# Kernel tuning notes

Hardware: AMD Instinct MI355X
Metric: run time of the kernel (lower is better)

The kernel has to match this reference:

```python
import jax, jax.numpy as jnp
import numpy as np

B, D_MODEL, D_MEM, H, N_MEM = 128, 1024, 64, 16, 4096


def setup_inputs() -> dict:
    key = jax.random.key(0)
    ks = jax.random.split(key, 6)
    scale = 1.0 / np.sqrt(D_MODEL)
    return {
        "query": jax.random.normal(ks[0], (B, D_MODEL), jnp.float32),
        "addresses": jax.random.normal(ks[1], (N_MEM, D_MEM), jnp.float32),
        "memories": jax.random.normal(ks[2], (B, N_MEM, D_MEM), jnp.float32),
        "Wq": jax.random.normal(ks[3], (D_MODEL, D_MODEL), jnp.float32) * scale,
        "bq": jnp.zeros((D_MODEL,), jnp.float32),
        "Wm": jax.random.normal(ks[4], (D_MODEL, D_MODEL), jnp.float32) * scale,
        "bm": jnp.zeros((D_MODEL,), jnp.float32),
    }


def reference(query, addresses, memories, Wq, bq, Wm, bm):
    # query projection -> heads: (B, H, d_mem)
    q = (query @ Wq.T + bq).reshape(B, H, D_MEM)
    # stage 1: build linear-attention kernel over the memory-slot dim
    k = jax.nn.relu(memories + addresses)            # (B, N, d_mem)
    matrix = jnp.einsum('bnd,bne->bde', k, memories)  # (B, d_mem, d_mem)
    normalizer = jnp.sum(k, axis=-2)                  # (B, d_mem)
    # stage 2: read the kernel with activated queries
    qa = jax.nn.relu(q)                               # (B, H, d_mem)
    numerator = jnp.einsum('bhd,bde->bhe', qa, matrix)
    denominator = jnp.einsum('bhd,bd->bh', qa, normalizer)[..., None] + 1e-5
    attn = numerator / denominator                    # (B, H, d_mem)
    return attn.reshape(B, H * D_MEM) @ Wm.T + bm     # (B, d_model)
```

## Files before the change

kernel.cpp:

```cpp
#include <hip/hip_runtime.h>
#include <hip/hip_bf16.h>

#define BATCH 128
#define DMEM 64
#define NMEM 4096
#define DMODEL 1024
#define S1 4
#define LDS_STRIDE 40

typedef __bf16 v8bf __attribute__((ext_vector_type(8)));
typedef __bf16 v2bf __attribute__((ext_vector_type(2)));
typedef float v4f __attribute__((ext_vector_type(4)));
typedef float v16f __attribute__((ext_vector_type(16)));

__device__ __forceinline__ void gemm_sk(const float* __restrict__ A,
                                        const float* __restrict__ W,
                                        float* __restrict__ dst,
                                        int m0, int n0, int k0,
                                        float* smem) {
    float(*As)[36] = (float(*)[36])smem;
    float(*Ws)[36] = (float(*)[36])(smem + 32 * 36);
    const int t = threadIdx.x;
    const int lrow = t >> 3;
    const int lc4 = (t & 7) * 4;
    const int rp = t >> 4;
    const int cp = t & 15;

    float acc00 = 0.f, acc01 = 0.f, acc10 = 0.f, acc11 = 0.f;

    v4f av = *(const v4f*)&A[(size_t)(m0 + lrow) * DMODEL + k0 + lc4];
    v4f wv = *(const v4f*)&W[(size_t)(n0 + lrow) * DMODEL + k0 + lc4];

    for (int c = 0; c < 4; ++c) {
        __syncthreads();
        *(v4f*)&As[lrow][lc4] = av;
        *(v4f*)&Ws[lrow][lc4] = wv;
        __syncthreads();
        if (c + 1 < 4) {
            const int kc = k0 + (c + 1) * 32;
            av = *(const v4f*)&A[(size_t)(m0 + lrow) * DMODEL + kc + lc4];
            wv = *(const v4f*)&W[(size_t)(n0 + lrow) * DMODEL + kc + lc4];
        }
#pragma unroll
        for (int kk = 0; kk < 32; kk += 4) {
            v4f a0 = *(v4f*)&As[rp][kk];
            v4f a1 = *(v4f*)&As[rp + 16][kk];
            v4f b0 = *(v4f*)&Ws[cp][kk];
            v4f b1 = *(v4f*)&Ws[cp + 16][kk];
#pragma unroll
            for (int q = 0; q < 4; ++q) {
                acc00 = fmaf(a0[q], b0[q], acc00);
                acc01 = fmaf(a0[q], b1[q], acc01);
                acc10 = fmaf(a1[q], b0[q], acc10);
                acc11 = fmaf(a1[q], b1[q], acc11);
            }
        }
    }
    dst[(size_t)(m0 + rp) * DMODEL + n0 + cp] = acc00;
    dst[(size_t)(m0 + rp) * DMODEL + n0 + cp + 16] = acc01;
    dst[(size_t)(m0 + rp + 16) * DMODEL + n0 + cp] = acc10;
    dst[(size_t)(m0 + rp + 16) * DMODEL + n0 + cp + 16] = acc11;
}

__global__ __launch_bounds__(256, 3) void k1(const float* __restrict__ mem,
                                             const float* __restrict__ addr,
                                             float* __restrict__ pmat,
                                             float* __restrict__ pnorm,
                                             const float* __restrict__ query,
                                             const float* __restrict__ Wq,
                                             float* __restrict__ qa_p) {
    __shared__ __align__(16) char smem[24576];
    const int bid = blockIdx.x;
    const int nst = BATCH * S1;

    if (bid >= nst) {
        const int b2 = bid - nst;
        const int m0 = (b2 & 3) * 32;
        const int n0 = ((b2 >> 2) & 31) * 32;
        const int ks = b2 >> 7;
        gemm_sk(query, Wq, qa_p + (size_t)ks * BATCH * DMODEL,
                m0, n0, ks * 128, (float*)smem);
        return;
    }

    float* norm_s = (float*)(smem + 20480);

    const int t = threadIdx.x;
    const int b = bid & (BATCH - 1);
    const int s = bid >> 7;
    const int slots_per = NMEM / S1;
    const int chunks = slots_per >> 5;

    const int u = t & 15;
    const int v = t >> 4;
    const int d0 = u * 4;

    const int l = t & 63;
    const int wv = t >> 6;
    const int strip = wv >> 1;
    const int kh = wv & 1;
    const int lrow = l & 31;
    const int lh = l >> 5;

    const size_t mem_base = ((size_t)b * NMEM + (size_t)s * slots_per) * DMEM;
    const size_t addr_base = (size_t)s * slots_per * DMEM;
    const size_t so = (size_t)(2 * v) * DMEM + d0;

    v16f acc0, acc1;
#pragma unroll
    for (int r = 0; r < 16; ++r) { acc0[r] = 0.f; acc1[r] = 0.f; }
    float nacc[4] = {0.f, 0.f, 0.f, 0.f};

    v4f mE0 = *(const v4f*)&mem[mem_base + so];
    v4f mE1 = *(const v4f*)&mem[mem_base + so + DMEM];
    v4f aE0 = *(const v4f*)&addr[addr_base + so];
    v4f aE1 = *(const v4f*)&addr[addr_base + so + DMEM];
    v4f mO0 = *(const v4f*)&mem[mem_base + 2048 + so];
    v4f mO1 = *(const v4f*)&mem[mem_base + 2048 + so + DMEM];
    v4f aO0 = *(const v4f*)&addr[addr_base + 2048 + so];
    v4f aO1 = *(const v4f*)&addr[addr_base + 2048 + so + DMEM];

    __bf16* kb0 = (__bf16*)smem;
    __bf16* mb0 = kb0 + 64 * LDS_STRIDE;
    __bf16* kb1 = (__bf16*)(smem + 10240);
    __bf16* mb1 = kb1 + 64 * LDS_STRIDE;
    const int cb = 16 * kh + 8 * lh;

    for (int cc = 0; cc < chunks; cc += 2) {
#pragma unroll
        for (int i = 0; i < 4; ++i) {
            float kf0 = fmaxf(mE0[i] + aE0[i], 0.f);
            float kf1 = fmaxf(mE1[i] + aE1[i], 0.f);
            nacc[i] += kf0 + kf1;
            v2bf kp; kp[0] = (__bf16)kf0; kp[1] = (__bf16)kf1;
            v2bf mp; mp[0] = (__bf16)mE0[i]; mp[1] = (__bf16)mE1[i];
            *(v2bf*)&kb0[(d0 + i) * LDS_STRIDE + 2 * v] = kp;
            *(v2bf*)&mb0[(d0 + i) * LDS_STRIDE + 2 * v] = mp;
        }
        if (cc + 2 < chunks) {
            const size_t coff = (size_t)(cc + 2) * 32 * DMEM;
            mE0 = *(const v4f*)&mem[mem_base + coff + so];
            mE1 = *(const v4f*)&mem[mem_base + coff + so + DMEM];
            aE0 = *(const v4f*)&addr[addr_base + coff + so];
            aE1 = *(const v4f*)&addr[addr_base + coff + so + DMEM];
        }
        __syncthreads();
        {
            v8bf af = *(v8bf*)&kb0[(32 * strip + lrow) * LDS_STRIDE + cb];
            v8bf b0 = *(v8bf*)&mb0[lrow * LDS_STRIDE + cb];
            v8bf b1 = *(v8bf*)&mb0[(32 + lrow) * LDS_STRIDE + cb];
            acc0 = __builtin_amdgcn_mfma_f32_32x32x16_bf16(af, b0, acc0, 0, 0, 0);
            acc1 = __builtin_amdgcn_mfma_f32_32x32x16_bf16(af, b1, acc1, 0, 0, 0);
        }
#pragma unroll
        for (int i = 0; i < 4; ++i) {
            float kf0 = fmaxf(mO0[i] + aO0[i], 0.f);
            float kf1 = fmaxf(mO1[i] + aO1[i], 0.f);
            nacc[i] += kf0 + kf1;
            v2bf kp; kp[0] = (__bf16)kf0; kp[1] = (__bf16)kf1;
            v2bf mp; mp[0] = (__bf16)mO0[i]; mp[1] = (__bf16)mO1[i];
            *(v2bf*)&kb1[(d0 + i) * LDS_STRIDE + 2 * v] = kp;
            *(v2bf*)&mb1[(d0 + i) * LDS_STRIDE + 2 * v] = mp;
        }
        if (cc + 3 < chunks) {
            const size_t coff = (size_t)(cc + 3) * 32 * DMEM;
            mO0 = *(const v4f*)&mem[mem_base + coff + so];
            mO1 = *(const v4f*)&mem[mem_base + coff + so + DMEM];
            aO0 = *(const v4f*)&addr[addr_base + coff + so];
            aO1 = *(const v4f*)&addr[addr_base + coff + so + DMEM];
        }
        __syncthreads();
        {
            v8bf af = *(v8bf*)&kb1[(32 * strip + lrow) * LDS_STRIDE + cb];
            v8bf b0 = *(v8bf*)&mb1[lrow * LDS_STRIDE + cb];
            v8bf b1 = *(v8bf*)&mb1[(32 + lrow) * LDS_STRIDE + cb];
            acc0 = __builtin_amdgcn_mfma_f32_32x32x16_bf16(af, b0, acc0, 0, 0, 0);
            acc1 = __builtin_amdgcn_mfma_f32_32x32x16_bf16(af, b1, acc1, 0, 0, 0);
        }
    }

    __syncthreads();
    float* red = (float*)smem;
#pragma unroll
    for (int i = 0; i < 4; ++i) norm_s[v * 64 + d0 + i] = nacc[i];
    if (kh == 1) {
#pragma unroll
        for (int r = 0; r < 16; ++r) {
            int row = (r & 3) + 8 * (r >> 2) + 4 * lh;
            int d = 32 * strip + row;
            red[lrow * 68 + d] = acc0[r];
            red[(32 + lrow) * 68 + d] = acc1[r];
        }
    }
    __syncthreads();
    if (kh == 0) {
#pragma unroll
        for (int r = 0; r < 16; ++r) {
            int row = (r & 3) + 8 * (r >> 2) + 4 * lh;
            int d = 32 * strip + row;
            red[lrow * 68 + d] += acc0[r];
            red[(32 + lrow) * 68 + d] += acc1[r];
        }
    }
    __syncthreads();
    {
        float* pm = pmat + ((size_t)s * BATCH + b) * 4096;
        const int e = t >> 2;
        const int ds = (t & 3) * 16;
#pragma unroll
        for (int j = 0; j < 4; ++j)
            *(v4f*)&pm[e * 64 + ds + 4 * j] = *(v4f*)&red[e * 68 + ds + 4 * j];
    }
    if (t < 64) {
        float ssum = 0.f;
#pragma unroll
        for (int g = 0; g < 16; ++g) ssum += norm_s[g * 64 + t];
        pnorm[((size_t)s * BATCH + b) * 64 + t] = ssum;
    }
}

__global__ __launch_bounds__(256) void stage2(const float* __restrict__ pmat,
                                              const float* __restrict__ pnorm,
                                              const float* __restrict__ qa_p,
                                              const float* __restrict__ bq,
                                              float* __restrict__ attn) {
    __shared__ float mat_s[16 * 68];
    __shared__ float qa_s[16 * 68];
    __shared__ float nrm_s[64];
    const int t = threadIdx.x;
    const int b = blockIdx.x >> 2;
    const int eq = blockIdx.x & 3;

    {
        const int i4 = t * 4;
        v4f acc = (v4f){0.f, 0.f, 0.f, 0.f};
#pragma unroll
        for (int s = 0; s < S1; ++s)
            acc += *(const v4f*)&pmat[((size_t)s * BATCH + b) * 4096 + eq * 1024 + i4];
        *(v4f*)&mat_s[(i4 >> 6) * 68 + (i4 & 63)] = acc;
    }
#pragma unroll
    for (int i = 0; i < 4; ++i) {
        const int idx = t + 256 * i;
        float ssum = 0.f;
#pragma unroll
        for (int ks = 0; ks < 8; ++ks)
            ssum += qa_p[((size_t)ks * BATCH + b) * DMODEL + idx];
        qa_s[(idx >> 6) * 68 + (idx & 63)] = fmaxf(ssum + bq[idx], 0.f);
    }
    if (t < 64) {
        float ssum = 0.f;
#pragma unroll
        for (int s = 0; s < S1; ++s)
            ssum += pnorm[((size_t)s * BATCH + b) * 64 + t];
        nrm_s[t] = ssum;
    }
    __syncthreads();

    const int h = t >> 4;
    const int e = t & 15;
    float num = 0.f, den = 0.f;
#pragma unroll 8
    for (int d = 0; d < 64; ++d) {
        float q = qa_s[h * 68 + d];
        num = fmaf(q, mat_s[e * 68 + d], num);
        den = fmaf(q, nrm_s[d], den);
    }
    attn[(size_t)b * DMODEL + h * 64 + eq * 16 + e] = num / (den + 1e-5f);
}

__global__ __launch_bounds__(256) void gemm_out(const float* __restrict__ A,
                                                const float* __restrict__ W,
                                                float* __restrict__ out_p) {
    __shared__ __align__(16) float smem[2 * 32 * 36];
    const int ks = blockIdx.z;
    gemm_sk(A, W, out_p + (size_t)ks * BATCH * DMODEL,
            blockIdx.x * 32, blockIdx.y * 32, ks * 128, smem);
}

__global__ __launch_bounds__(256) void combine(const float* __restrict__ out_p,
                                               const float* __restrict__ bm,
                                               float* __restrict__ out) {
    const int i = blockIdx.x * 256 + threadIdx.x;
    float ssum = bm[i & (DMODEL - 1)];
#pragma unroll
    for (int ks = 0; ks < 8; ++ks)
        ssum += out_p[(size_t)ks * BATCH * DMODEL + i];
    out[i] = ssum;
}

extern "C" void kernel_launch(void* const* d_in, const int* in_sizes, int n_in,
                              void* d_out, int out_size, void* d_ws, size_t ws_size,
                              hipStream_t stream) {
    const float* query     = (const float*)d_in[0];
    const float* addresses = (const float*)d_in[1];
    const float* memories  = (const float*)d_in[2];
    const float* Wq        = (const float*)d_in[3];
    const float* bq        = (const float*)d_in[4];
    const float* Wm        = (const float*)d_in[5];
    const float* bm        = (const float*)d_in[6];
    float* out = (float*)d_out;
    float* ws = (float*)d_ws;

    float* qa_p    = ws;
    float* attn_ws = qa_p + 1048576;
    float* pnorm   = attn_ws + 131072;
    float* pmat    = pnorm + 32768;
    float* out_p   = pmat + 2097152;

    k1<<<dim3(BATCH * S1 + 1024), 256, 0, stream>>>(memories, addresses, pmat,
                                                    pnorm, query, Wq, qa_p);
    stage2<<<dim3(512), 256, 0, stream>>>(pmat, pnorm, qa_p, bq, attn_ws);
    gemm_out<<<dim3(4, 32, 8), 256, 0, stream>>>(attn_ws, Wm, out_p);
    combine<<<dim3(512), 256, 0, stream>>>(out_p, bm, out);
}
```

Measured before the change: 226.8 us.

## Use 64x64 register-tiled GEMM, drop split-K for query projection, fuse bias+relu

Replaces the 32x32 tile GEMM helper with a 64x64 tile, 4x4 per-thread register-blocked version that double-buffers LDS across two chunk buffers. The query projection inside k1 now runs as 32 full-K blocks that write qa directly with bias and ReLU applied, instead of 1024 split-K blocks writing 8 partial sums that stage2 had to reduce. The output GEMM uses the same helper with fewer, larger blocks. This cuts partial-sum traffic and raises arithmetic intensity. The cost is that the projection now sits on only 32 long full-K blocks, which may lengthen k1's tail, and k1 needs more LDS per block.

```diff
diff --git a/kernel.cpp b/kernel.cpp
--- a/kernel.cpp
+++ b/kernel.cpp
@@ -13,53 +13,101 @@
 typedef float v4f __attribute__((ext_vector_type(4)));
 typedef float v16f __attribute__((ext_vector_type(16)));
 
-__device__ __forceinline__ void gemm_sk(const float* __restrict__ A,
-                                        const float* __restrict__ W,
-                                        float* __restrict__ dst,
-                                        int m0, int n0, int k0,
-                                        float* smem) {
-    float(*As)[36] = (float(*)[36])smem;
-    float(*Ws)[36] = (float(*)[36])(smem + 32 * 36);
+__device__ __forceinline__ void gemm64(const float* __restrict__ A,
+                                       const float* __restrict__ W,
+                                       const float* __restrict__ bias,
+                                       float* __restrict__ dst,
+                                       int m0, int n0, int k0, int nchunks,
+                                       int relu, float* smem) {
+    float* As0 = smem;
+    float* Ws0 = smem + 64 * 36;
+    float* As1 = smem + 2 * 64 * 36;
+    float* Ws1 = smem + 3 * 64 * 36;
     const int t = threadIdx.x;
-    const int lrow = t >> 3;
-    const int lc4 = (t & 7) * 4;
+    const int lrow = t >> 2;
+    const int lc8 = (t & 3) * 8;
     const int rp = t >> 4;
     const int cp = t & 15;
 
-    float acc00 = 0.f, acc01 = 0.f, acc10 = 0.f, acc11 = 0.f;
-
-    v4f av = *(const v4f*)&A[(size_t)(m0 + lrow) * DMODEL + k0 + lc4];
-    v4f wv = *(const v4f*)&W[(size_t)(n0 + lrow) * DMODEL + k0 + lc4];
-
-    for (int c = 0; c < 4; ++c) {
+    float acc[4][4];
+#pragma unroll
+    for (int i = 0; i < 4; ++i)
+#pragma unroll
+        for (int j = 0; j < 4; ++j) acc[i][j] = 0.f;
+
+    const float* Arow = A + (size_t)(m0 + lrow) * DMODEL + lc8;
+    const float* Wrow = W + (size_t)(n0 + lrow) * DMODEL + lc8;
+
+    v4f aE0 = *(const v4f*)&Arow[k0];
+    v4f aE1 = *(const v4f*)&Arow[k0 + 4];
+    v4f wE0 = *(const v4f*)&Wrow[k0];
+    v4f wE1 = *(const v4f*)&Wrow[k0 + 4];
+    v4f aO0 = *(const v4f*)&Arow[k0 + 32];
+    v4f aO1 = *(const v4f*)&Arow[k0 + 36];
+    v4f wO0 = *(const v4f*)&Wrow[k0 + 32];
+    v4f wO1 = *(const v4f*)&Wrow[k0 + 36];
+
+    for (int cc = 0; cc < nchunks; cc += 2) {
+        *(v4f*)&As0[lrow * 36 + lc8] = aE0;
+        *(v4f*)&As0[lrow * 36 + lc8 + 4] = aE1;
+        *(v4f*)&Ws0[lrow * 36 + lc8] = wE0;
+        *(v4f*)&Ws0[lrow * 36 + lc8 + 4] = wE1;
+        if (cc + 2 < nchunks) {
+            const int kc = k0 + (cc + 2) * 32;
+            aE0 = *(const v4f*)&Arow[kc]; aE1 = *(const v4f*)&Arow[kc + 4];
+            wE0 = *(const v4f*)&Wrow[kc]; wE1 = *(const v4f*)&Wrow[kc + 4];
+        }
         __syncthreads();
-        *(v4f*)&As[lrow][lc4] = av;
-        *(v4f*)&Ws[lrow][lc4] = wv;
+#pragma unroll
+        for (int kk = 0; kk < 32; kk += 4) {
+            v4f a[4], b[4];
+#pragma unroll
+            for (int i = 0; i < 4; ++i) a[i] = *(v4f*)&As0[(rp + 16 * i) * 36 + kk];
+#pragma unroll
+            for (int j = 0; j < 4; ++j) b[j] = *(v4f*)&Ws0[(cp + 16 * j) * 36 + kk];
+#pragma unroll
+            for (int i = 0; i < 4; ++i)
+#pragma unroll
+                for (int j = 0; j < 4; ++j)
+#pragma unroll
+                    for (int q = 0; q < 4; ++q)
+                        acc[i][j] = fmaf(a[i][q], b[j][q], acc[i][j]);
+        }
+        *(v4f*)&As1[lrow * 36 + lc8] = aO0;
+        *(v4f*)&As1[lrow * 36 + lc8 + 4] = aO1;
+        *(v4f*)&Ws1[lrow * 36 + lc8] = wO0;
+        *(v4f*)&Ws1[lrow * 36 + lc8 + 4] = wO1;
+        if (cc + 3 < nchunks) {
+            const int kc = k0 + (cc + 3) * 32;
+            aO0 = *(const v4f*)&Arow[kc]; aO1 = *(const v4f*)&Arow[kc + 4];
+            wO0 = *(const v4f*)&Wrow[kc]; wO1 = *(const v4f*)&Wrow[kc + 4];
+        }
         __syncthreads();
-        if (c + 1 < 4) {
-            const int kc = k0 + (c + 1) * 32;
-            av = *(const v4f*)&A[(size_t)(m0 + lrow) * DMODEL + kc + lc4];
-            wv = *(const v4f*)&W[(size_t)(n0 + lrow) * DMODEL + kc + lc4];
-        }
 #pragma unroll
         for (int kk = 0; kk < 32; kk += 4) {
-            v4f a0 = *(v4f*)&As[rp][kk];
-            v4f a1 = *(v4f*)&As[rp + 16][kk];
-            v4f b0 = *(v4f*)&Ws[cp][kk];
-            v4f b1 = *(v4f*)&Ws[cp + 16][kk];
-#pragma unroll
-            for (int q = 0; q < 4; ++q) {
-                acc00 = fmaf(a0[q], b0[q], acc00);
-                acc01 = fmaf(a0[q], b1[q], acc01);
-                acc10 = fmaf(a1[q], b0[q], acc10);
-                acc11 = fmaf(a1[q], b1[q], acc11);
-            }
-        }
-    }
-    dst[(size_t)(m0 + rp) * DMODEL + n0 + cp] = acc00;
-    dst[(size_t)(m0 + rp) * DMODEL + n0 + cp + 16] = acc01;
-    dst[(size_t)(m0 + rp + 16) * DMODEL + n0 + cp] = acc10;
-    dst[(size_t)(m0 + rp + 16) * DMODEL + n0 + cp + 16] = acc11;
+            v4f a[4], b[4];
+#pragma unroll
+            for (int i = 0; i < 4; ++i) a[i] = *(v4f*)&As1[(rp + 16 * i) * 36 + kk];
+#pragma unroll
+            for (int j = 0; j < 4; ++j) b[j] = *(v4f*)&Ws1[(cp + 16 * j) * 36 + kk];
+#pragma unroll
+            for (int i = 0; i < 4; ++i)
+#pragma unroll
+                for (int j = 0; j < 4; ++j)
+#pragma unroll
+                    for (int q = 0; q < 4; ++q)
+                        acc[i][j] = fmaf(a[i][q], b[j][q], acc[i][j]);
+        }
+    }
+
+#pragma unroll
+    for (int i = 0; i < 4; ++i)
+#pragma unroll
+        for (int j = 0; j < 4; ++j) {
+            float o = acc[i][j] + (bias ? bias[n0 + cp + 16 * j] : 0.f);
+            if (relu) o = fmaxf(o, 0.f);
+            dst[(size_t)(m0 + rp + 16 * i) * DMODEL + n0 + cp + 16 * j] = o;
+        }
 }
 
 __global__ __launch_bounds__(256, 3) void k1(const float* __restrict__ mem,
@@ -68,18 +116,16 @@
                                              float* __restrict__ pnorm,
                                              const float* __restrict__ query,
                                              const float* __restrict__ Wq,
-                                             float* __restrict__ qa_p) {
-    __shared__ __align__(16) char smem[24576];
+                                             const float* __restrict__ bq,
+                                             float* __restrict__ qa) {
+    __shared__ __align__(16) char smem[36864];
     const int bid = blockIdx.x;
     const int nst = BATCH * S1;
 
     if (bid >= nst) {
         const int b2 = bid - nst;
-        const int m0 = (b2 & 3) * 32;
-        const int n0 = ((b2 >> 2) & 31) * 32;
-        const int ks = b2 >> 7;
-        gemm_sk(query, Wq, qa_p + (size_t)ks * BATCH * DMODEL,
-                m0, n0, ks * 128, (float*)smem);
+        gemm64(query, Wq, bq, qa, (b2 & 1) * 64, (b2 >> 1) * 64, 0, 32, 1,
+               (float*)smem);
         return;
     }
 
@@ -221,8 +267,7 @@
 
 __global__ __launch_bounds__(256) void stage2(const float* __restrict__ pmat,
                                               const float* __restrict__ pnorm,
-                                              const float* __restrict__ qa_p,
-                                              const float* __restrict__ bq,
+                                              const float* __restrict__ qa,
                                               float* __restrict__ attn) {
     __shared__ float mat_s[16 * 68];
     __shared__ float qa_s[16 * 68];
@@ -242,11 +287,7 @@
 #pragma unroll
     for (int i = 0; i < 4; ++i) {
         const int idx = t + 256 * i;
-        float ssum = 0.f;
-#pragma unroll
-        for (int ks = 0; ks < 8; ++ks)
-            ssum += qa_p[((size_t)ks * BATCH + b) * DMODEL + idx];
-        qa_s[(idx >> 6) * 68 + (idx & 63)] = fmaxf(ssum + bq[idx], 0.f);
+        qa_s[(idx >> 6) * 68 + (idx & 63)] = qa[(size_t)b * DMODEL + idx];
     }
     if (t < 64) {
         float ssum = 0.f;
@@ -272,10 +313,10 @@
 __global__ __launch_bounds__(256) void gemm_out(const float* __restrict__ A,
                                                 const float* __restrict__ W,
                                                 float* __restrict__ out_p) {
-    __shared__ __align__(16) float smem[2 * 32 * 36];
+    __shared__ __align__(16) float smem[4 * 64 * 36];
     const int ks = blockIdx.z;
-    gemm_sk(A, W, out_p + (size_t)ks * BATCH * DMODEL,
-            blockIdx.x * 32, blockIdx.y * 32, ks * 128, smem);
+    gemm64(A, W, nullptr, out_p + (size_t)ks * BATCH * DMODEL,
+           blockIdx.x * 64, blockIdx.y * 64, ks * 128, 4, 0, smem);
 }
 
 __global__ __launch_bounds__(256) void combine(const float* __restrict__ out_p,
@@ -302,15 +343,15 @@
     float* out = (float*)d_out;
     float* ws = (float*)d_ws;
 
-    float* qa_p    = ws;
-    float* attn_ws = qa_p + 1048576;
+    float* qa      = ws;
+    float* attn_ws = qa + 131072;
     float* pnorm   = attn_ws + 131072;
     float* pmat    = pnorm + 32768;
     float* out_p   = pmat + 2097152;
 
-    k1<<<dim3(BATCH * S1 + 1024), 256, 0, stream>>>(memories, addresses, pmat,
-                                                    pnorm, query, Wq, qa_p);
-    stage2<<<dim3(512), 256, 0, stream>>>(pmat, pnorm, qa_p, bq, attn_ws);
-    gemm_out<<<dim3(4, 32, 8), 256, 0, stream>>>(attn_ws, Wm, out_p);
+    k1<<<dim3(BATCH * S1 + 32), 256, 0, stream>>>(memories, addresses, pmat,
+                                                  pnorm, query, Wq, bq, qa);
+    stage2<<<dim3(512), 256, 0, stream>>>(pmat, pnorm, qa, attn_ws);
+    gemm_out<<<dim3(2, 16, 8), 256, 0, stream>>>(attn_ws, Wm, out_p);
     combine<<<dim3(512), 256, 0, stream>>>(out_p, bm, out);
 }
```

Result: slower. 411.0 us (+81.2%).
